# Kernel optimization log

Hardware: AMD Instinct MI355X
Metric: run time of the kernel (lower is better)

The kernel has to match this reference:

```python
import jax, jax.numpy as jnp
import numpy as np
from jax import lax

# 2D MPS-RNN (one-site, hilbert_local=2, real params, snake order, 'regular' phase)
# Faithful reconstruction of MPS_RNN_2D forward: site-by-site recurrence over an
# L x M lattice. At each site: candidate hidden states for both local occupations
#   h_cand[s] = M_h[i,j,s] @ h_left + M_v[i,j,s] @ h_below + v[i,j,s]
# conditional prob p(s) ~ sum_d eta[i,j,d]^2 * h_cand[s,d]^2 (eta-weighted norm),
# selected hidden state is renormalized; phase accumulates arg(w.h + c) (0 or pi
# for real params). Returns [B,2]: (log|psi|, phase).

L, M, S, D = 8, 8, 2, 32   # rows, cols, local Hilbert dim, bond dim dcut
B = 32768                  # batch of sampled configurations
NQ = L * M                 # nqubits
EPS = 1e-10


def setup_inputs() -> dict:
    key = jax.random.key(0)
    ks = jax.random.split(key, 7)
    sc = np.float32(1.0 / np.sqrt(D))  # keep hidden-state norms O(1)
    x = jax.random.randint(ks[0], (B, NQ), 0, 2, dtype=jnp.int32)
    M_h = jax.random.normal(ks[1], (L, M, S, D, D), jnp.float32) * sc
    M_v = jax.random.normal(ks[2], (L, M, S, D, D), jnp.float32) * sc
    v = jax.random.normal(ks[3], (L, M, S, D), jnp.float32) * sc
    w = jax.random.normal(ks[4], (L, M, D), jnp.float32) * sc
    c = jnp.zeros((L, M), jnp.float32)
    eta = jax.random.normal(ks[5], (L, M, D), jnp.float32)
    return {"x": x, "M_h": M_h, "M_v": M_v, "v": v, "w": w, "c": c, "eta": eta}


def _forward(x, M_h, M_v, v, w, c, eta):
    dt = M_h.dtype
    # snake order: odd rows are scanned right-to-left in lattice coordinates.
    cols = jnp.arange(M)
    odd = (jnp.arange(L) % 2 == 1)[:, None]
    colmap = jnp.where(odd, M - 1 - cols[None, :], cols[None, :])  # [L,M] scan-pos -> lattice col (involution)
    ri = jnp.arange(L)[:, None]
    gather = lambda p: p[ri, colmap]  # reorder params into scan order per row
    M_h_s, M_v_s, v_s, w_s, c_s, eta_s = (gather(p) for p in (M_h, M_v, v, w, c, eta))
    x_s = x.reshape(B, L, M).transpose(1, 2, 0)  # [L,M,B] already in qubit/scan order

    pi_f = jnp.asarray(np.pi, dt)

    def col_step(h_h, cin):
        Mh, Mv, vv, ww, cc, ee, xx, hv = cin
        # candidate states for both local occupations: [B,S,D]
        hc = (jnp.einsum('sab,Bb->Bsa', Mh, h_h)
              + jnp.einsum('sab,Bb->Bsa', Mv, hv)
              + vv[None])
        p = jnp.einsum('Bsa,a->Bs', hc * hc, ee * ee)  # eta-weighted squared norms
        psel = jnp.take_along_axis(p, xx[:, None], axis=1)[:, 0]
        dla = 0.5 * (jnp.log(psel + EPS) - jnp.log(p.sum(-1) + EPS))
        hsel = jnp.take_along_axis(hc, xx[:, None, None], axis=1)[:, 0]  # [B,D]
        hn = hsel / (jnp.sqrt(jnp.sum(hsel * hsel, -1, keepdims=True)) + EPS)
        a = hn @ ww + cc  # [B]
        dph = jnp.where(a < 0, pi_f, jnp.asarray(0, dt))  # arg of real scalar
        return hn, (dla, dph, hn)

    def row_step(carry, rin):
        h_v_lat, la, ph = carry
        Mh_r, Mv_r, v_r, w_r, c_r, e_r, x_r, cmap = rin
        hv_scan = h_v_lat[:, cmap].transpose(1, 0, 2)  # [M,B,D] vertical inputs in scan order
        h0 = jnp.ones((B, D), dt)  # left_boundary = ones
        _, (dlas, dphs, hs) = lax.scan(col_step, h0, (Mh_r, Mv_r, v_r, w_r, c_r, e_r, x_r, hv_scan))
        la = la + dlas.sum(0)
        ph = ph + dphs.sum(0)
        h_new = hs.transpose(1, 0, 2)[:, cmap]  # back to lattice column order (cmap is an involution)
        return (h_new, la, ph), None

    init = (jnp.zeros((B, M, D), dt),  # bottom_boundary = zeros
            jnp.zeros((B,), dt), jnp.zeros((B,), dt))
    (hv, log_amp, phase), _ = lax.scan(row_step, init, (M_h_s, M_v_s, v_s, w_s, c_s, eta_s, x_s, colmap))
    return jnp.stack([log_amp, phase], axis=-1)  # [B,2]


def reference(x, M_h, M_v, v, w, c, eta):
    return _forward(x, M_h, M_v, v, w, c, eta)
```

## Files before the change

kernel.cpp:

```cpp
#include <hip/hip_runtime.h>

#define LROWS 8
#define MCOLS 8
#define BD 32
#define NSITE 64
#define SPB 64
#define BTOT 32768
#define NBLK (BTOT / SPB)
#define EPS 1e-10
#define PI_D 3.14159265358979323846

#define W_OFF 0
#define CB_OFF 262144
#define CC_OFF (262144 + 12288)
#define WS_DBLS (CC_OFF + 64)

__global__ void precompute_kernel(const float* __restrict__ M_h,
                                  const float* __restrict__ M_v,
                                  const float* __restrict__ v,
                                  const float* __restrict__ w,
                                  const float* __restrict__ cc,
                                  const float* __restrict__ eta,
                                  double* __restrict__ ws) {
    int idx = blockIdx.x * 256 + threadIdx.x;
    if (idx >= WS_DBLS) return;
    double val = 0.0;
    if (idx < CB_OFF) {
        int pair = idx & 1, a8 = (idx >> 1) & 7, b = (idx >> 4) & 31;
        int r = (idx >> 9) & 7, site = idx >> 12;
        int i = site >> 3, js = site & 7;
        int c = (i & 1) ? (MCOLS - 1 - js) : js;
        int s = r >> 2, a = (r & 3) * 8 + a8;
        if (pair == 0) val = (double)M_h[(((i * MCOLS + c) * 2 + s) * BD + a) * BD + b];
        else           val = (double)M_v[(((i * MCOLS + c) * 2 + s) * BD + a) * BD + b];
    } else if (idx < CC_OFF) {
        int j = idx - CB_OFF;
        int site = j / 192;
        int rem = j - site * 192;
        int r = rem / 24, t = rem - r * 24;
        int i = site >> 3, js = site & 7;
        int c = (i & 1) ? (MCOLS - 1 - js) : js;
        int s = r >> 2, a0 = (r & 3) * 8;
        if (t < 8)       val = (double)v[(((i * MCOLS + c) * 2 + s) * BD) + a0 + t];
        else if (t < 16) { double e = (double)eta[(i * MCOLS + c) * BD + a0 + (t - 8)]; val = e * e; }
        else             val = (double)w[(i * MCOLS + c) * BD + a0 + (t - 16)];
    } else {
        int site = idx - CC_OFF;
        int i = site >> 3, js = site & 7;
        int c = (i & 1) ? (MCOLS - 1 - js) : js;
        val = (double)cc[i * MCOLS + c];
    }
    ws[idx] = val;
}

__launch_bounds__(512, 2)
__global__ void mps_main_kernel(const int* __restrict__ x,
                                const double* __restrict__ ws,
                                float* __restrict__ out) {
    __shared__ double hRow[MCOLS][BD][SPB];
    __shared__ double hOnes[BD][SPB];
    __shared__ double pbuf[8][SPB];
    __shared__ double ssb[8][SPB];
    __shared__ double phb[8][SPB];

    const int tid = threadIdx.x;
    const int k = tid & 63;
    const int r = tid >> 6;
    const int r_u = __builtin_amdgcn_readfirstlane(r);
    const int s = r_u >> 2;
    const int abase = (r_u & 3) * 8;
    const long kg = (long)blockIdx.x * SPB + k;

    for (int t = tid; t < MCOLS * BD * SPB; t += 512) (&hRow[0][0][0])[t] = 0.0;
    for (int t = tid; t < BD * SPB; t += 512) (&hOnes[0][0])[t] = 1.0;
    __syncthreads();

    const double2* __restrict__ Wp = (const double2*)ws;

    double la = 0.0, ph = 0.0;
    double2 wreg[2][16];

    {
        const double2* __restrict__ w0 = Wp + (size_t)(0 * 8 + r_u) * 256;
        #pragma unroll
        for (int t = 0; t < 16; ++t) wreg[0][t] = w0[t];
    }

    for (int i = 0; i < LROWS; ++i) {
        const int* xp = x + kg * NSITE + i * MCOLS;
        int4 xa = *reinterpret_cast<const int4*>(xp);
        int4 xb = *reinterpret_cast<const int4*>(xp + 4);
        const unsigned xbits = (unsigned)((xa.x & 1)        | ((xa.y & 1) << 1) |
                                          ((xa.z & 1) << 2) | ((xa.w & 1) << 3) |
                                          ((xb.x & 1) << 4) | ((xb.y & 1) << 5) |
                                          ((xb.z & 1) << 6) | ((xb.w & 1) << 7));
        double prodN = 1.0, prodD = 1.0;

        for (int js = 0; js < MCOLS; ++js) {
            const int site = i * MCOLS + js;
            const int c = (i & 1) ? (MCOLS - 1 - js) : js;
            const int cprev = (i & 1) ? (MCOLS - js) : (js - 1);

            const double2* __restrict__ wsite = Wp + (size_t)(site * 8 + r_u) * 256;
            const double*  __restrict__ cb    = ws + CB_OFF + (size_t)(site * 8 + r_u) * 24;

            const double* __restrict__ colV = &hRow[c][0][0];
            const double* __restrict__ colL = (js == 0) ? &hOnes[0][0] : &hRow[cprev][0][0];

            double acc[8];
            #pragma unroll
            for (int a = 0; a < 8; ++a) acc[a] = 0.0;

            #pragma unroll
            for (int bb = 0; bb < 16; ++bb) {
                const int cur = bb & 1;
                if (bb < 15) {
                    const double2* __restrict__ wn = wsite + (bb + 1) * 16;
                    #pragma unroll
                    for (int t = 0; t < 16; ++t) wreg[cur ^ 1][t] = wn[t];
                }
                #pragma unroll
                for (int bq = 0; bq < 2; ++bq) {
                    const int b = bb * 2 + bq;
                    const double hlb = colL[b * SPB + k];
                    const double hvb = colV[b * SPB + k];
                    #pragma unroll
                    for (int a = 0; a < 8; ++a) {
                        const double2 w2 = wreg[cur][bq * 8 + a];
                        acc[a] = fma(w2.x, hlb, fma(w2.y, hvb, acc[a]));
                    }
                }
            }
            #pragma unroll
            for (int a = 0; a < 8; ++a) acc[a] += cb[a];

            double pp = 0.0, ssp = 0.0, php = 0.0;
            #pragma unroll
            for (int a = 0; a < 8; ++a) {
                const double t2 = acc[a] * acc[a];
                pp  = fma(t2, cb[8 + a], pp);
                ssp += t2;
                php = fma(acc[a], cb[16 + a], php);
            }
            const double ccoef = ws[CC_OFF + site];
            const int xs = (int)((xbits >> js) & 1u);
            const bool sel = (s == xs);

            pbuf[r][k] = pp;
            ssb[r][k]  = ssp;
            phb[r][k]  = php;
            __syncthreads();

            {
                const double2* __restrict__ wn = Wp + (size_t)((site + 1) * 8 + r_u) * 256;
                #pragma unroll
                for (int t = 0; t < 16; ++t) wreg[0][t] = wn[t];
            }

            const double p0 = ((pbuf[0][k] + pbuf[1][k]) + pbuf[2][k]) + pbuf[3][k];
            const double p1 = ((pbuf[4][k] + pbuf[5][k]) + pbuf[6][k]) + pbuf[7][k];
            const double psel = xs ? p1 : p0;
            prodN *= (psel + EPS);
            prodD *= (p0 + p1 + EPS);

            const int gb = xs * 4;
            const double ss = ((ssb[gb][k] + ssb[gb + 1][k]) + ssb[gb + 2][k]) + ssb[gb + 3][k];
            const double inv = 1.0 / (sqrt(ss) + EPS);
            if (sel) {
                #pragma unroll
                for (int a = 0; a < 8; ++a)
                    hRow[c][abase + a][k] = acc[a] * inv;
            }
            const double phd = ((phb[gb][k] + phb[gb + 1][k]) + phb[gb + 2][k]) + phb[gb + 3][k];
            const double aph = phd * inv + ccoef;
            ph += (aph < 0.0) ? PI_D : 0.0;

            __syncthreads();
        }
        la += 0.5 * (log(prodN) - log(prodD));
    }

    if (r == 0) {
        out[kg * 2]     = (float)la;
        out[kg * 2 + 1] = (float)ph;
    }
}

extern "C" void kernel_launch(void* const* d_in, const int* in_sizes, int n_in,
                              void* d_out, int out_size, void* d_ws, size_t ws_size,
                              hipStream_t stream) {
    const int*   x    = (const int*)d_in[0];
    const float* M_h  = (const float*)d_in[1];
    const float* M_v  = (const float*)d_in[2];
    const float* v    = (const float*)d_in[3];
    const float* w    = (const float*)d_in[4];
    const float* cc   = (const float*)d_in[5];
    const float* eta  = (const float*)d_in[6];
    float* out = (float*)d_out;
    double* ws = (double*)d_ws;

    const int pre_total = WS_DBLS;
    dim3 preGrid((pre_total + 255) / 256), preBlock(256);
    hipLaunchKernelGGL(precompute_kernel, preGrid, preBlock, 0, stream,
                       M_h, M_v, v, w, cc, eta, ws);

    dim3 grid(NBLK), block(512);
    hipLaunchKernelGGL(mps_main_kernel, grid, block, 0, stream, x, ws, out);
}
```

Measured before the change: 707.7 us.

## Specialize left-boundary column, shrink reduction buffers, defer probability bookkeeping to wave 0

Removes the ones-filled shared buffer by specializing the js==0 step so the left-boundary contribution is a plain add of the weight. Reduction buffers shrink: probabilities are stored as float, and only the selected state's waves write norm and phase partials. The probability and phase accumulation moves after the second barrier, runs only in wave 0, and uses double-buffered slots. Launch bounds drop to one block per CU, and the float probability partials lower the precision of the log-amplitude.

```diff
diff --git a/kernel.cpp b/kernel.cpp
--- a/kernel.cpp
+++ b/kernel.cpp
@@ -53,15 +53,14 @@
     ws[idx] = val;
 }
 
-__launch_bounds__(512, 2)
+__launch_bounds__(512, 1)
 __global__ void mps_main_kernel(const int* __restrict__ x,
                                 const double* __restrict__ ws,
                                 float* __restrict__ out) {
     __shared__ double hRow[MCOLS][BD][SPB];
-    __shared__ double hOnes[BD][SPB];
-    __shared__ double pbuf[8][SPB];
-    __shared__ double ssb[8][SPB];
-    __shared__ double phb[8][SPB];
+    __shared__ float  pbuf[2][8][SPB];
+    __shared__ double ssb[4][SPB];
+    __shared__ double phb[2][4][SPB];
 
     const int tid = threadIdx.x;
     const int k = tid & 63;
@@ -69,19 +68,21 @@
     const int r_u = __builtin_amdgcn_readfirstlane(r);
     const int s = r_u >> 2;
     const int abase = (r_u & 3) * 8;
+    const int j4 = r_u & 3;
     const long kg = (long)blockIdx.x * SPB + k;
 
     for (int t = tid; t < MCOLS * BD * SPB; t += 512) (&hRow[0][0][0])[t] = 0.0;
-    for (int t = tid; t < BD * SPB; t += 512) (&hOnes[0][0])[t] = 1.0;
     __syncthreads();
 
     const double2* __restrict__ Wp = (const double2*)ws;
 
     double la = 0.0, ph = 0.0;
+    double prodN = 1.0, prodD = 1.0;
+    int par = 0;
     double2 wreg[2][16];
 
     {
-        const double2* __restrict__ w0 = Wp + (size_t)(0 * 8 + r_u) * 256;
+        const double2* __restrict__ w0 = Wp + (size_t)r_u * 256;
         #pragma unroll
         for (int t = 0; t < 16; ++t) wreg[0][t] = w0[t];
     }
@@ -94,7 +95,7 @@
                                           ((xa.z & 1) << 2) | ((xa.w & 1) << 3) |
                                           ((xb.x & 1) << 4) | ((xb.y & 1) << 5) |
                                           ((xb.z & 1) << 6) | ((xb.w & 1) << 7));
-        double prodN = 1.0, prodD = 1.0;
+        prodN = 1.0; prodD = 1.0;
 
         for (int js = 0; js < MCOLS; ++js) {
             const int site = i * MCOLS + js;
@@ -105,29 +106,51 @@
             const double*  __restrict__ cb    = ws + CB_OFF + (size_t)(site * 8 + r_u) * 24;
 
             const double* __restrict__ colV = &hRow[c][0][0];
-            const double* __restrict__ colL = (js == 0) ? &hOnes[0][0] : &hRow[cprev][0][0];
 
             double acc[8];
             #pragma unroll
             for (int a = 0; a < 8; ++a) acc[a] = 0.0;
 
-            #pragma unroll
-            for (int bb = 0; bb < 16; ++bb) {
-                const int cur = bb & 1;
-                if (bb < 15) {
-                    const double2* __restrict__ wn = wsite + (bb + 1) * 16;
+            if (js == 0) {
+                #pragma unroll
+                for (int bb = 0; bb < 16; ++bb) {
+                    const int cur = bb & 1;
+                    if (bb < 15) {
+                        const double2* __restrict__ wn = wsite + (bb + 1) * 16;
+                        #pragma unroll
+                        for (int t = 0; t < 16; ++t) wreg[cur ^ 1][t] = wn[t];
+                    }
                     #pragma unroll
-                    for (int t = 0; t < 16; ++t) wreg[cur ^ 1][t] = wn[t];
+                    for (int bq = 0; bq < 2; ++bq) {
+                        const int b = bb * 2 + bq;
+                        const double hvb = colV[b * SPB + k];
+                        #pragma unroll
+                        for (int a = 0; a < 8; ++a) {
+                            const double2 w2 = wreg[cur][bq * 8 + a];
+                            acc[a] = fma(w2.y, hvb, acc[a] + w2.x);
+                        }
+                    }
                 }
-                #pragma unroll
-                for (int bq = 0; bq < 2; ++bq) {
-                    const int b = bb * 2 + bq;
-                    const double hlb = colL[b * SPB + k];
-                    const double hvb = colV[b * SPB + k];
+            } else {
+                const double* __restrict__ colL = &hRow[cprev][0][0];
+                #pragma unroll
+                for (int bb = 0; bb < 16; ++bb) {
+                    const int cur = bb & 1;
+                    if (bb < 15) {
+                        const double2* __restrict__ wn = wsite + (bb + 1) * 16;
+                        #pragma unroll
+                        for (int t = 0; t < 16; ++t) wreg[cur ^ 1][t] = wn[t];
+                    }
                     #pragma unroll
-                    for (int a = 0; a < 8; ++a) {
-                        const double2 w2 = wreg[cur][bq * 8 + a];
-                        acc[a] = fma(w2.x, hlb, fma(w2.y, hvb, acc[a]));
+                    for (int bq = 0; bq < 2; ++bq) {
+                        const int b = bb * 2 + bq;
+                        const double hlb = colL[b * SPB + k];
+                        const double hvb = colV[b * SPB + k];
+                        #pragma unroll
+                        for (int a = 0; a < 8; ++a) {
+                            const double2 w2 = wreg[cur][bq * 8 + a];
+                            acc[a] = fma(w2.x, hlb, fma(w2.y, hvb, acc[a]));
+                        }
                     }
                 }
             }
@@ -146,9 +169,8 @@
             const int xs = (int)((xbits >> js) & 1u);
             const bool sel = (s == xs);
 
-            pbuf[r][k] = pp;
-            ssb[r][k]  = ssp;
-            phb[r][k]  = php;
+            pbuf[par][r][k] = (float)pp;
+            if (sel) { ssb[j4][k] = ssp; phb[par][j4][k] = php; }
             __syncthreads();
 
             {
@@ -157,27 +179,29 @@
                 for (int t = 0; t < 16; ++t) wreg[0][t] = wn[t];
             }
 
-            const double p0 = ((pbuf[0][k] + pbuf[1][k]) + pbuf[2][k]) + pbuf[3][k];
-            const double p1 = ((pbuf[4][k] + pbuf[5][k]) + pbuf[6][k]) + pbuf[7][k];
-            const double psel = xs ? p1 : p0;
-            prodN *= (psel + EPS);
-            prodD *= (p0 + p1 + EPS);
-
-            const int gb = xs * 4;
-            const double ss = ((ssb[gb][k] + ssb[gb + 1][k]) + ssb[gb + 2][k]) + ssb[gb + 3][k];
+            const double ss = (ssb[0][k] + ssb[1][k]) + (ssb[2][k] + ssb[3][k]);
             const double inv = 1.0 / (sqrt(ss) + EPS);
             if (sel) {
                 #pragma unroll
                 for (int a = 0; a < 8; ++a)
                     hRow[c][abase + a][k] = acc[a] * inv;
             }
-            const double phd = ((phb[gb][k] + phb[gb + 1][k]) + phb[gb + 2][k]) + phb[gb + 3][k];
-            const double aph = phd * inv + ccoef;
-            ph += (aph < 0.0) ? PI_D : 0.0;
-
             __syncthreads();
+
+            if (r_u == 0) {
+                const float* __restrict__ pb = &pbuf[par][0][0];
+                const double p0 = (double)((pb[0*SPB+k] + pb[1*SPB+k]) + (pb[2*SPB+k] + pb[3*SPB+k]));
+                const double p1 = (double)((pb[4*SPB+k] + pb[5*SPB+k]) + (pb[6*SPB+k] + pb[7*SPB+k]));
+                const double psel = xs ? p1 : p0;
+                prodN *= (psel + EPS);
+                prodD *= (p0 + p1 + EPS);
+                const double phd = (phb[par][0][k] + phb[par][1][k]) + (phb[par][2][k] + phb[par][3][k]);
+                const double aph = phd * inv + ccoef;
+                ph += (aph < 0.0) ? PI_D : 0.0;
+            }
+            par ^= 1;
         }
-        la += 0.5 * (log(prodN) - log(prodD));
+        if (r_u == 0) la += 0.5 * (log(prodN) - log(prodD));
     }
 
     if (r == 0) {
```

After: 1.352 ms. 91.0% more time.
